# Performance work log

Measured on AMD Instinct MI355X. Metric: run time of the kernel, lower is better.

## Reference

```python
import jax, jax.numpy as jnp
import numpy as np

INPUT_SIZE = 64
HIDDEN = 16
BATCH = 1048576


def setup_inputs() -> dict:
    key = jax.random.key(0)
    ks = jax.random.split(key, 16)
    D = INPUT_SIZE + HIDDEN
    s = 1.0 / np.sqrt(D)  # torch nn.Linear default init scale
    inp = {
        "x": jax.random.normal(ks[0], (BATCH, INPUT_SIZE), jnp.float32),
        "h_prev": jax.random.normal(ks[1], (BATCH, HIDDEN), jnp.float32),
        "c_prev": jax.random.normal(ks[2], (BATCH, HIDDEN), jnp.float32),
        "delta_t": jax.random.uniform(ks[3], (BATCH,), jnp.float32),
    }
    names = ["i", "f", "o", "c", "d"]
    for j, n in enumerate(names):
        inp[f"W_{n}"] = jax.random.uniform(ks[4 + 2 * j], (D, HIDDEN), jnp.float32, -s, s)
        inp[f"b_{n}"] = jax.random.uniform(ks[5 + 2 * j], (HIDDEN,), jnp.float32, -s, s)
    return inp


def reference(x, h_prev, c_prev, delta_t, W_i, b_i, W_f, b_f, W_o, b_o, W_c, b_c, W_d, b_d):
    combined = jnp.concatenate([x, h_prev], axis=1)  # [B, D]
    # Fuse the five small GEMMs into one [D, 5H] GEMM (same math).
    W = jnp.concatenate([W_i, W_f, W_o, W_c, W_d], axis=1)  # [D, 5H]
    b = jnp.concatenate([b_i, b_f, b_o, b_c, b_d])  # [5H]
    z = combined @ W + b  # [B, 5H]
    zi, zf, zo, zc, zd = jnp.split(z, 5, axis=1)
    i = jnp.tanh(zi)
    f = jnp.tanh(zf)
    o = jnp.tanh(zo)
    c_tilde = jnp.tanh(zc)
    decay = jax.nn.softplus(zd)
    c_decay = c_prev * jnp.exp(-decay * delta_t[:, None])
    c_next = f * c_decay + i * c_tilde
    h_next = o * jnp.tanh(c_next)
    return (h_next, c_next)
```

## Files before the change

### kernel.cpp

```cpp
#include <hip/hip_runtime.h>


#define BATCH   1048576
#define NTILES  (BATCH / 16)
#define L2E     1.442695041f
#define LN2     0.6931471806f

typedef __bf16 bf16x8 __attribute__((ext_vector_type(8)));
typedef float  f32x4  __attribute__((ext_vector_type(4)));

__device__ __forceinline__ float fast_tanh(float x) {
    float e = __builtin_amdgcn_exp2f(x * (2.0f * L2E));
    return 1.0f - 2.0f * __builtin_amdgcn_rcpf(e + 1.0f);
}

__device__ __forceinline__ bf16x8 pack_bf16(float4 lo, float4 hi) {
    bf16x8 r;
    r[0] = (__bf16)lo.x; r[1] = (__bf16)lo.y; r[2] = (__bf16)lo.z; r[3] = (__bf16)lo.w;
    r[4] = (__bf16)hi.x; r[5] = (__bf16)hi.y; r[6] = (__bf16)hi.z; r[7] = (__bf16)hi.w;
    return r;
}

__global__ __launch_bounds__(256, 3)
void ctlstm_kernel(const float* __restrict__ x,
                   const float* __restrict__ hprev,
                   const float* __restrict__ cprev,
                   const float* __restrict__ dt,
                   const float* __restrict__ Wi, const float* __restrict__ bi,
                   const float* __restrict__ Wf, const float* __restrict__ bf_,
                   const float* __restrict__ Wo, const float* __restrict__ bo,
                   const float* __restrict__ Wc, const float* __restrict__ bc,
                   const float* __restrict__ Wd, const float* __restrict__ bd,
                   float* __restrict__ out)
{
    const int lane = threadIdx.x & 63;
    const int col  = lane & 15;
    const int quad = lane >> 4;

    const float* W[5]  = {Wi, Wf, Wo, Wc, Wd};
    const float* BP[5] = {bi, bf_, bo, bc, bd};

    bf16x8 Bfrag[3][5];
    float  biasv[5];
    #pragma unroll
    for (int t = 0; t < 5; ++t) {
        biasv[t] = BP[t][col];
        #pragma unroll
        for (int kt = 0; kt < 3; ++kt) {
            bf16x8 f;
            #pragma unroll
            for (int j = 0; j < 8; ++j) {
                int k = kt * 32 + quad * 8 + j;
                float v = (k < 80) ? W[t][k * 16 + col] : 0.0f;
                f[j] = (__bf16)v;
            }
            Bfrag[kt][t] = f;
        }
    }

    const int nwaves = (gridDim.x * blockDim.x) >> 6;
    const int gw     = (blockIdx.x * blockDim.x + threadIdx.x) >> 6;

    const float4* X4 = (const float4*)x;
    const float4* H4 = (const float4*)hprev;

    for (int tile = gw; tile < NTILES; tile += nwaves) {
        const int rowbase = tile << 4;
        const int arow    = rowbase + col;

        float4 a0 = X4[arow * 16 + quad * 2];
        float4 a1 = X4[arow * 16 + quad * 2 + 1];
        float4 a2 = X4[arow * 16 + 8 + quad * 2];
        float4 a3 = X4[arow * 16 + 8 + quad * 2 + 1];
        float4 a4 = make_float4(0.f, 0.f, 0.f, 0.f);
        float4 a5 = make_float4(0.f, 0.f, 0.f, 0.f);
        if (quad < 2) {
            a4 = H4[arow * 4 + quad * 2];
            a5 = H4[arow * 4 + quad * 2 + 1];
        }
        bf16x8 A0 = pack_bf16(a0, a1);
        bf16x8 A1 = pack_bf16(a2, a3);
        bf16x8 A2 = pack_bf16(a4, a5);

        f32x4 acc[5];
        #pragma unroll
        for (int t = 0; t < 5; ++t) {
            f32x4 c0 = {biasv[t], biasv[t], biasv[t], biasv[t]};
            c0 = __builtin_amdgcn_mfma_f32_16x16x32_bf16(A0, Bfrag[0][t], c0, 0, 0, 0);
            c0 = __builtin_amdgcn_mfma_f32_16x16x32_bf16(A1, Bfrag[1][t], c0, 0, 0, 0);
            acc[t] = __builtin_amdgcn_mfma_f32_16x16x32_bf16(A2, Bfrag[2][t], c0, 0, 0, 0);
        }

        #pragma unroll
        for (int r = 0; r < 4; ++r) {
            const int row = rowbase + quad * 4 + r;
            float cp  = cprev[row * 16 + col];
            float dtv = dt[row];

            float zi = acc[0][r], zf = acc[1][r], zo = acc[2][r];
            float zc = acc[3][r], zd = acc[4][r];

            float i_g = fast_tanh(zi);
            float f_g = fast_tanh(zf);
            float o_g = fast_tanh(zo);
            float ctl = fast_tanh(zc);

            float ax = fabsf(zd);
            float e  = __builtin_amdgcn_exp2f(-ax * L2E);
            float sp = fmaxf(zd, 0.0f) + __builtin_amdgcn_logf(1.0f + e) * LN2;

            float cdec = cp * __builtin_amdgcn_exp2f(-sp * dtv * L2E);
            float cn   = f_g * cdec + i_g * ctl;
            float hn   = o_g * fast_tanh(cn);

            out[row * 16 + col]              = hn;
            out[BATCH * 16 + row * 16 + col] = cn;
        }
    }
}

extern "C" void kernel_launch(void* const* d_in, const int* in_sizes, int n_in,
                              void* d_out, int out_size, void* d_ws, size_t ws_size,
                              hipStream_t stream) {
    const float* x  = (const float*)d_in[0];
    const float* h  = (const float*)d_in[1];
    const float* c  = (const float*)d_in[2];
    const float* dt = (const float*)d_in[3];
    ctlstm_kernel<<<1024, 256, 0, stream>>>(
        x, h, c, dt,
        (const float*)d_in[4],  (const float*)d_in[5],
        (const float*)d_in[6],  (const float*)d_in[7],
        (const float*)d_in[8],  (const float*)d_in[9],
        (const float*)d_in[10], (const float*)d_in[11],
        (const float*)d_in[12], (const float*)d_in[13],
        (float*)d_out);
}
```

Measured before the change: 524.1 us.

## Prepack weights in a separate kernel, hoist c_prev loads, use nontemporal stores

Adds a small pre-kernel that converts the five weight matrices into bf16 MFMA fragments and biases in the workspace, so each wave loads pre-packed fragments instead of doing strided fp32 gathers and conversions. The main kernel also issues the c_prev and delta_t loads before the MFMAs to overlap their latency, writes outputs with nontemporal stores, raises the occupancy hint to 4 blocks per SM, and launches 8192 blocks instead of 1024. The extra launch adds some fixed overhead, and the larger grid means per-wave weight setup is repeated more often.

```diff
diff --git a/kernel.cpp b/kernel.cpp
--- a/kernel.cpp
+++ b/kernel.cpp
@@ -9,53 +9,65 @@
 typedef __bf16 bf16x8 __attribute__((ext_vector_type(8)));
 typedef float  f32x4  __attribute__((ext_vector_type(4)));
 
+#define WS_BIAS_OFF 15360
+
 __device__ __forceinline__ float fast_tanh(float x) {
     float e = __builtin_amdgcn_exp2f(x * (2.0f * L2E));
     return 1.0f - 2.0f * __builtin_amdgcn_rcpf(e + 1.0f);
 }
 
-__device__ __forceinline__ bf16x8 pack_bf16(float4 lo, float4 hi) {
-    bf16x8 r;
-    r[0] = (__bf16)lo.x; r[1] = (__bf16)lo.y; r[2] = (__bf16)lo.z; r[3] = (__bf16)lo.w;
-    r[4] = (__bf16)hi.x; r[5] = (__bf16)hi.y; r[6] = (__bf16)hi.z; r[7] = (__bf16)hi.w;
-    return r;
+__global__ void pack_w_kernel(const float* __restrict__ Wi, const float* __restrict__ bi,
+                              const float* __restrict__ Wf, const float* __restrict__ bf_,
+                              const float* __restrict__ Wo, const float* __restrict__ bo,
+                              const float* __restrict__ Wc, const float* __restrict__ bc,
+                              const float* __restrict__ Wd, const float* __restrict__ bd,
+                              void* __restrict__ ws)
+{
+    const float* W[5]  = {Wi, Wf, Wo, Wc, Wd};
+    const float* BP[5] = {bi, bf_, bo, bc, bd};
+    const int b    = blockIdx.x;
+    const int lane = threadIdx.x;
+    if (b < 15) {
+        const int t = b / 3, kt = b % 3;
+        const int quad = lane >> 4, col = lane & 15;
+        bf16x8 f;
+        #pragma unroll
+        for (int j = 0; j < 8; ++j) {
+            int k = kt * 32 + quad * 8 + j;
+            float v = (k < 80) ? W[t][k * 16 + col] : 0.0f;
+            f[j] = (__bf16)v;
+        }
+        ((bf16x8*)ws)[b * 64 + lane] = f;
+    } else {
+        if (lane < 80) {
+            int t = lane >> 4, col = lane & 15;
+            ((float*)((char*)ws + WS_BIAS_OFF))[lane] = BP[t][col];
+        }
+    }
 }
 
-__global__ __launch_bounds__(256, 3)
+__global__ __launch_bounds__(256, 4)
 void ctlstm_kernel(const float* __restrict__ x,
                    const float* __restrict__ hprev,
                    const float* __restrict__ cprev,
                    const float* __restrict__ dt,
-                   const float* __restrict__ Wi, const float* __restrict__ bi,
-                   const float* __restrict__ Wf, const float* __restrict__ bf_,
-                   const float* __restrict__ Wo, const float* __restrict__ bo,
-                   const float* __restrict__ Wc, const float* __restrict__ bc,
-                   const float* __restrict__ Wd, const float* __restrict__ bd,
+                   const void* __restrict__ ws,
                    float* __restrict__ out)
 {
     const int lane = threadIdx.x & 63;
     const int col  = lane & 15;
     const int quad = lane >> 4;
 
-    const float* W[5]  = {Wi, Wf, Wo, Wc, Wd};
-    const float* BP[5] = {bi, bf_, bo, bc, bd};
-
+    const bf16x8* wsfrag = (const bf16x8*)ws;
+    const float*  wsbias = (const float*)((const char*)ws + WS_BIAS_OFF);
     bf16x8 Bfrag[3][5];
     float  biasv[5];
     #pragma unroll
     for (int t = 0; t < 5; ++t) {
-        biasv[t] = BP[t][col];
+        biasv[t] = wsbias[t * 16 + col];
         #pragma unroll
-        for (int kt = 0; kt < 3; ++kt) {
-            bf16x8 f;
-            #pragma unroll
-            for (int j = 0; j < 8; ++j) {
-                int k = kt * 32 + quad * 8 + j;
-                float v = (k < 80) ? W[t][k * 16 + col] : 0.0f;
-                f[j] = (__bf16)v;
-            }
-            Bfrag[kt][t] = f;
-        }
+        for (int kt = 0; kt < 3; ++kt)
+            Bfrag[kt][t] = wsfrag[(t * 3 + kt) * 64 + lane];
     }
 
     const int nwaves = (gridDim.x * blockDim.x) >> 6;
@@ -78,9 +90,25 @@
             a4 = H4[arow * 4 + quad * 2];
             a5 = H4[arow * 4 + quad * 2 + 1];
         }
-        bf16x8 A0 = pack_bf16(a0, a1);
-        bf16x8 A1 = pack_bf16(a2, a3);
-        bf16x8 A2 = pack_bf16(a4, a5);
+
+        float cp[4], dtv[4];
+        #pragma unroll
+        for (int r = 0; r < 4; ++r) {
+            const int row = rowbase + quad * 4 + r;
+            cp[r]  = cprev[row * 16 + col];
+            dtv[r] = dt[row];
+        }
+
+        bf16x8 A0, A1, A2;
+        #pragma unroll
+        for (int j = 0; j < 4; ++j) {
+            A0[j]     = (__bf16)((const float*)&a0)[j];
+            A0[j + 4] = (__bf16)((const float*)&a1)[j];
+            A1[j]     = (__bf16)((const float*)&a2)[j];
+            A1[j + 4] = (__bf16)((const float*)&a3)[j];
+            A2[j]     = (__bf16)((const float*)&a4)[j];
+            A2[j + 4] = (__bf16)((const float*)&a5)[j];
+        }
 
         f32x4 acc[5];
         #pragma unroll
@@ -94,8 +122,6 @@
         #pragma unroll
         for (int r = 0; r < 4; ++r) {
             const int row = rowbase + quad * 4 + r;
-            float cp  = cprev[row * 16 + col];
-            float dtv = dt[row];
 
             float zi = acc[0][r], zf = acc[1][r], zo = acc[2][r];
             float zc = acc[3][r], zd = acc[4][r];
@@ -109,12 +135,12 @@
             float e  = __builtin_amdgcn_exp2f(-ax * L2E);
             float sp = fmaxf(zd, 0.0f) + __builtin_amdgcn_logf(1.0f + e) * LN2;
 
-            float cdec = cp * __builtin_amdgcn_exp2f(-sp * dtv * L2E);
+            float cdec = cp[r] * __builtin_amdgcn_exp2f(-sp * dtv[r] * L2E);
             float cn   = f_g * cdec + i_g * ctl;
             float hn   = o_g * fast_tanh(cn);
 
-            out[row * 16 + col]              = hn;
-            out[BATCH * 16 + row * 16 + col] = cn;
+            __builtin_nontemporal_store(hn, &out[row * 16 + col]);
+            __builtin_nontemporal_store(cn, &out[BATCH * 16 + row * 16 + col]);
         }
     }
 }
@@ -122,16 +148,15 @@
 extern "C" void kernel_launch(void* const* d_in, const int* in_sizes, int n_in,
                               void* d_out, int out_size, void* d_ws, size_t ws_size,
                               hipStream_t stream) {
-    const float* x  = (const float*)d_in[0];
-    const float* h  = (const float*)d_in[1];
-    const float* c  = (const float*)d_in[2];
-    const float* dt = (const float*)d_in[3];
-    ctlstm_kernel<<<1024, 256, 0, stream>>>(
-        x, h, c, dt,
+    pack_w_kernel<<<16, 64, 0, stream>>>(
         (const float*)d_in[4],  (const float*)d_in[5],
         (const float*)d_in[6],  (const float*)d_in[7],
         (const float*)d_in[8],  (const float*)d_in[9],
         (const float*)d_in[10], (const float*)d_in[11],
         (const float*)d_in[12], (const float*)d_in[13],
-        (float*)d_out);
+        d_ws);
+    ctlstm_kernel<<<8192, 256, 0, stream>>>(
+        (const float*)d_in[0], (const float*)d_in[1],
+        (const float*)d_in[2], (const float*)d_in[3],
+        d_ws, (float*)d_out);
 }
```

Result: faster. 510.1 us (-2.7%).
